# Kernel tuning notes

Hardware: AMD Instinct MI355X
Metric: run time of the kernel (lower is better)

Reference implementation:

```python
import jax, jax.numpy as jnp
import numpy as np

K = 7          # kernel_size
PAD = K // 2   # padding


def _unfold(t):
    """im2col for kxk neighborhood: (B,C,H,W) -> (B,C,K*K,H,W), zero-padded."""
    B, C, H, W = t.shape
    p = jnp.pad(t, ((0, 0), (0, 0), (PAD, PAD), (PAD, PAD)))
    # row-major over kernel offsets matches F.unfold ordering
    wins = jnp.stack([p[:, :, i:i + H, j:j + W]
                      for i in range(K) for j in range(K)], axis=2)
    return wins


def setup_inputs() -> dict:
    key = jax.random.key(0)
    ks = jax.random.split(key, 7)
    B, C, H, W = 8, 128, 64, 64
    scale = 1.0 / np.sqrt(C)
    x = jax.random.normal(ks[0], (B, C, H, W), dtype=jnp.float32)
    Wq = jax.random.normal(ks[1], (C, C), dtype=jnp.float32) * scale
    Wk = jax.random.normal(ks[2], (C, C), dtype=jnp.float32) * scale
    Wv = jax.random.normal(ks[3], (C, C), dtype=jnp.float32) * scale
    bq = jax.random.normal(ks[4], (C,), dtype=jnp.float32) * 0.01
    bk = jax.random.normal(ks[5], (C,), dtype=jnp.float32) * 0.01
    bv = jax.random.normal(ks[6], (C,), dtype=jnp.float32) * 0.01
    return {"x": x, "Wq": Wq, "bq": bq, "Wk": Wk, "bk": bk, "Wv": Wv, "bv": bv}


def reference(x, Wq, bq, Wk, bk, Wv, bv):
    # 1x1 convs = channel GEMMs
    q = jnp.einsum('oc,bchw->bohw', Wq, x) + bq[:, None, None]
    k = jnp.einsum('oc,bchw->bohw', Wk, x) + bk[:, None, None]
    v = jnp.einsum('oc,bchw->bohw', Wv, x) + bv[:, None, None]
    k_unf = _unfold(k)   # (B,C,K*K,H,W)
    v_unf = _unfold(v)   # (B,C,K*K,H,W)
    # attention scores over the K*K neighborhood, summed over channels
    attn = jnp.einsum('bchw,bcphw->bphw', q, k_unf)
    attn = jax.nn.softmax(attn, axis=1)
    y = jnp.einsum('bphw,bcphw->bchw', attn, v_unf)
    return y
```

## Files before the change

### kernel.cpp

```cpp
#include <hip/hip_runtime.h>
#include <hip/hip_bf16.h>

#define CC   128
#define HH_  64
#define WW_  64
#define BB   8
#define HWSZ (HH_*WW_)
#define CHW  (CC*HWSZ)
#define BCHW (BB*CHW)
#define PAD  3
#define NP   49

typedef __attribute__((ext_vector_type(8))) short short8;
typedef __attribute__((ext_vector_type(4))) float float4v;

__global__ __launch_bounds__(256) void prep_w(
    const float* __restrict__ Wq, const float* __restrict__ Wk,
    const float* __restrict__ Wv,
    unsigned short* __restrict__ whi, unsigned short* __restrict__ wlo)
{
    int i = blockIdx.x * 256 + threadIdx.x;
    const float* src = (i < 16384) ? Wq : (i < 32768 ? Wk : Wv);
    float f = src[i & 16383];
    __hip_bfloat16 h = __float2bfloat16(f);
    float hf = __bfloat162float(h);
    __hip_bfloat16 l = __float2bfloat16(f - hf);
    unsigned short hu, lu;
    __builtin_memcpy(&hu, &h, 2);
    __builtin_memcpy(&lu, &l, 2);
    whi[i] = hu;
    wlo[i] = lu;
}

__global__ __launch_bounds__(256, 2) void qkv_mfma(
    const float* __restrict__ x,
    const unsigned short* __restrict__ whi, const unsigned short* __restrict__ wlo,
    const float* __restrict__ bq, const float* __restrict__ bk,
    const float* __restrict__ bv, float* __restrict__ qkv)
{
    __shared__ unsigned short xT[2][128][136];
    const int proj = blockIdx.y;
    const int n0g  = blockIdx.x << 7;
    const int b    = n0g >> 12;
    const int npx  = n0g & 4095;
    const int tid  = threadIdx.x;
    const int lane = tid & 63;
    const int wv   = tid >> 6;
    const int wm   = wv & 1, wn = wv >> 1;

    const float* xb = x + (size_t)b*CHW + npx;
    #pragma unroll
    for (int it = 0; it < 16; ++it) {
        int f  = tid + (it << 8);
        int c  = f >> 5;
        int p4 = (f & 31) << 2;
        float4 v = *(const float4*)&xb[(size_t)c*HWSZ + p4];
        float vv[4] = {v.x, v.y, v.z, v.w};
        #pragma unroll
        for (int u = 0; u < 4; ++u) {
            __hip_bfloat16 h = __float2bfloat16(vv[u]);
            float hf = __bfloat162float(h);
            __hip_bfloat16 l = __float2bfloat16(vv[u] - hf);
            unsigned short hu, lu;
            __builtin_memcpy(&hu, &h, 2);
            __builtin_memcpy(&lu, &l, 2);
            xT[0][p4 + u][c] = hu;
            xT[1][p4 + u][c] = lu;
        }
    }

    const float* Bp = (proj == 0) ? bq : (proj == 1 ? bk : bv);
    const int q4 = lane >> 4;
    float4v acc[4][4];
    #pragma unroll
    for (int sm = 0; sm < 4; ++sm) {
        const int mb = wm*64 + sm*16 + q4*4;
        float4v bi;
        bi[0] = Bp[mb+0]; bi[1] = Bp[mb+1]; bi[2] = Bp[mb+2]; bi[3] = Bp[mb+3];
        #pragma unroll
        for (int sn = 0; sn < 4; ++sn) acc[sm][sn] = bi;
    }

    __syncthreads();

    const unsigned short* Wh = whi + (size_t)proj*16384;
    const unsigned short* Wl = wlo + (size_t)proj*16384;
    const int kq8  = q4 << 3;
    const int mrow = lane & 15;

    for (int pass = 0; pass < 3; ++pass) {
        const unsigned short* Wp = (pass == 2) ? Wl : Wh;
        const int xi = (pass == 1) ? 1 : 0;
        #pragma unroll
        for (int kc = 0; kc < 4; ++kc) {
            const int kb = kc << 5;
            short8 a[4], bf[4];
            #pragma unroll
            for (int sm = 0; sm < 4; ++sm) {
                const int m = wm*64 + sm*16 + mrow;
                a[sm] = *(const short8*)&Wp[(size_t)m*CC + kb + kq8];
            }
            #pragma unroll
            for (int sn = 0; sn < 4; ++sn) {
                const int n = wn*64 + sn*16 + mrow;
                bf[sn] = *(const short8*)&xT[xi][n][kb + kq8];
            }
            #pragma unroll
            for (int sm = 0; sm < 4; ++sm)
                #pragma unroll
                for (int sn = 0; sn < 4; ++sn)
                    acc[sm][sn] = __builtin_amdgcn_mfma_f32_16x16x32_bf16(
                        a[sm], bf[sn], acc[sm][sn], 0, 0, 0);
        }
    }

    float* op = qkv + (size_t)proj*BCHW + (size_t)b*CHW + npx;
    #pragma unroll
    for (int sm = 0; sm < 4; ++sm) {
        const int mb = wm*64 + sm*16 + q4*4;
        #pragma unroll
        for (int sn = 0; sn < 4; ++sn) {
            const int n = wn*64 + sn*16 + mrow;
            #pragma unroll
            for (int r = 0; r < 4; ++r)
                op[(size_t)(mb + r)*HWSZ + n] = acc[sm][sn][r];
        }
    }
}

__device__ __forceinline__ void load_chunk8(const float* __restrict__ src,
                                            int h0, int c0, float4* stg) {
    const int tid = threadIdx.x;
    #pragma unroll
    for (int i = 0; i < 4; ++i) {
        int f   = tid + (i << 9);
        int c   = f >> 7;
        int rem = f & 127;
        int r   = rem >> 4;
        int q4  = (rem & 15) << 2;
        int hh  = h0 - PAD + r;
        if ((unsigned)hh < (unsigned)HH_)
            stg[i] = *(const float4*)&src[(size_t)(c0 + c)*HWSZ + hh*WW_ + q4];
        else
            stg[i] = make_float4(0.f, 0.f, 0.f, 0.f);
    }
}

__global__ __launch_bounds__(512) void locatt(
    const float* __restrict__ qkv, float* __restrict__ out)
{
    __shared__ __align__(16) float smem[8*72*17];
    __shared__ float lg[2][NP][64];
    __shared__ float dn[2][64];

    const int blk = blockIdx.x;
    const int xs  = blk & 7;
    const int jj  = blk >> 3;
    const int b   = jj >> 2;
    const int h0  = (((xs << 2) | (jj & 3)) << 1);
    const int tid = threadIdx.x;
    const int s   = tid >> 6;
    const int lane = tid & 63;
    const int q16  = lane & 15;
    const int csub = lane >> 4;
    const int w4   = q16 << 2;
    const int w    = lane;

    const float* qp = qkv + (size_t)b*CHW;
    const float* kp = qkv + (size_t)BCHW + (size_t)b*CHW;
    const float* vp = qkv + (size_t)2*BCHW + (size_t)b*CHW;

    float (*ks)[8][72] = (float(*)[8][72])smem;

    if (tid < 256) {
        int idx = tid & 127;
        int c = idx >> 3, r = idx & 7;
        int col = (tid < 128) ? 0 : 68;
        *(float4*)&ks[c][r][col] = make_float4(0.f, 0.f, 0.f, 0.f);
    }

    const bool do0 = (s < 7);
    const bool do1 = (s >= 1);

    float acc0[7][4], acc1[7][4];
    #pragma unroll
    for (int dx = 0; dx < 7; ++dx)
        #pragma unroll
        for (int j = 0; j < 4; ++j) { acc0[dx][j] = 0.f; acc1[dx][j] = 0.f; }

    float4 stg[4];
    load_chunk8(kp, h0, 0, stg);

    for (int ck = 0; ck < 8; ++ck) {
        #pragma unroll
        for (int i = 0; i < 4; ++i) {
            int f   = tid + (i << 9);
            int c   = f >> 7;
            int rem = f & 127;
            int r   = rem >> 4;
            int q4  = (rem & 15) << 2;
            *(float4*)&ks[c][r][4 + q4] = stg[i];
        }
        __syncthreads();
        if (ck < 7) load_chunk8(kp, h0, (ck + 1) * 16, stg);

        const int c0 = ck << 4;
        #pragma unroll
        for (int ci4 = 0; ci4 < 4; ++ci4) {
            const int c = (ci4 << 2) + csub;
            const float* qc = qp + (size_t)(c0 + c)*HWSZ + h0*WW_ + w4;
            float4 q0v = do0 ? *(const float4*)qc
                             : make_float4(0.f, 0.f, 0.f, 0.f);
            float4 q1v = do1 ? *(const float4*)(qc + WW_)
                             : make_float4(0.f, 0.f, 0.f, 0.f);
            float4 ka  = *(const float4*)&ks[c][s][w4];
            float4 kb  = *(const float4*)&ks[c][s][w4 + 4];
            float4 kc2 = *(const float4*)&ks[c][s][w4 + 8];
            float kw[12] = {ka.x,ka.y,ka.z,ka.w, kb.x,kb.y,kb.z,kb.w,
                            kc2.x,kc2.y,kc2.z,kc2.w};
            float q0a[4] = {q0v.x,q0v.y,q0v.z,q0v.w};
            float q1a[4] = {q1v.x,q1v.y,q1v.z,q1v.w};
            #pragma unroll
            for (int dx = 0; dx < 7; ++dx)
                #pragma unroll
                for (int j = 0; j < 4; ++j) {
                    float kv = kw[j + dx + 1];
                    acc0[dx][j] = fmaf(q0a[j], kv, acc0[dx][j]);
                    acc1[dx][j] = fmaf(q1a[j], kv, acc1[dx][j]);
                }
        }
        __syncthreads();
    }

    #pragma unroll
    for (int dx = 0; dx < 7; ++dx)
        #pragma unroll
        for (int j = 0; j < 4; ++j) {
            acc0[dx][j] += __shfl_xor(acc0[dx][j], 16, 64);
            acc0[dx][j] += __shfl_xor(acc0[dx][j], 32, 64);
            acc1[dx][j] += __shfl_xor(acc1[dx][j], 16, 64);
            acc1[dx][j] += __shfl_xor(acc1[dx][j], 32, 64);
        }
    #pragma unroll
    for (int dx = 0; dx < 7; ++dx) {
        if ((dx & 3) == csub) {
            if (do0) *(float4*)&lg[0][s*7 + dx][w4] =
                make_float4(acc0[dx][0], acc0[dx][1], acc0[dx][2], acc0[dx][3]);
            if (do1) *(float4*)&lg[1][(s-1)*7 + dx][w4] =
                make_float4(acc1[dx][0], acc1[dx][1], acc1[dx][2], acc1[dx][3]);
        }
    }

    float vreg[16];
    {
        #pragma unroll
        for (int i = 0; i < 16; ++i) {
            int c  = 2*s + (i >> 3);
            int r  = i & 7;
            int hh = h0 - PAD + r;
            vreg[i] = ((unsigned)hh < (unsigned)HH_)
                      ? vp[(size_t)c*HWSZ + hh*WW_ + w] : 0.f;
        }
    }
    __syncthreads();

    if (tid < 128) {
        const int r = tid >> 6, px = tid & 63;
        float tv[NP];
        float m = -1e30f;
        #pragma unroll
        for (int p = 0; p < NP; ++p) { tv[p] = lg[r][p][px]; m = fmaxf(m, tv[p]); }
        float d = 0.f;
        #pragma unroll
        for (int p = 0; p < NP; ++p) {
            float e = __expf(tv[p] - m);
            d += e;
            lg[r][p][px] = e;
        }
        dn[r][px] = 1.f / d;
    } else {
        int t = tid - 128;
        for (int i = t; i < 1024; i += 384) {
            int r    = i >> 7;
            int rem  = i & 127;
            int colg = rem >> 4;
            int col  = (colg < 4) ? colg : (64 + colg);
            smem[r*1224 + col*17 + (rem & 15)] = 0.f;
        }
    }
    __syncthreads();

    float a0[NP], a1[NP];
    const float sc0 = dn[0][w], sc1 = dn[1][w];
    #pragma unroll
    for (int p = 0; p < NP; ++p) a0[p] = lg[0][p][w] * sc0;
    #pragma unroll
    for (int p = 0; p < NP; ++p) a1[p] = lg[1][p][w] * sc1;

    for (int ck = 0; ck < 8; ++ck) {
        #pragma unroll
        for (int i = 0; i < 16; ++i) {
            int c = 2*s + (i >> 3);
            int r = i & 7;
            smem[r*1224 + (4 + w)*17 + c] = vreg[i];
        }
        __syncthreads();
        if (ck < 7) {
            int c0v = (ck + 1) << 4;
            #pragma unroll
            for (int i = 0; i < 16; ++i) {
                int c  = 2*s + (i >> 3);
                int r  = i & 7;
                int hh = h0 - PAD + r;
                vreg[i] = ((unsigned)hh < (unsigned)HH_)
                          ? vp[(size_t)(c0v + c)*HWSZ + hh*WW_ + w] : 0.f;
            }
        }
        float y0a = 0.f, y0b = 0.f, y1a = 0.f, y1b = 0.f;
        #pragma unroll
        for (int r = 0; r < 8; ++r) {
            const float* vbase = &smem[r*1224 + (1 + w)*17 + 2*s];
            #pragma unroll
            for (int dx = 0; dx < 7; ++dx) {
                float va = vbase[17*dx];
                float vb = vbase[17*dx + 1];
                if (r < 7) {
                    float aw = a0[r*7 + dx];
                    y0a = fmaf(aw, va, y0a); y0b = fmaf(aw, vb, y0b);
                }
                if (r >= 1) {
                    float aw = a1[(r-1)*7 + dx];
                    y1a = fmaf(aw, va, y1a); y1b = fmaf(aw, vb, y1b);
                }
            }
        }
        float* op = out + (size_t)b*CHW + (size_t)(ck*16 + 2*s)*HWSZ
                        + (size_t)h0*WW_ + w;
        op[0]          = y0a;
        op[WW_]        = y1a;
        op[HWSZ]       = y0b;
        op[HWSZ + WW_] = y1b;
        __syncthreads();
    }
}

extern "C" void kernel_launch(void* const* d_in, const int* in_sizes, int n_in,
                              void* d_out, int out_size, void* d_ws, size_t ws_size,
                              hipStream_t stream) {
    const float* x  = (const float*)d_in[0];
    const float* Wq = (const float*)d_in[1];
    const float* bq = (const float*)d_in[2];
    const float* Wk = (const float*)d_in[3];
    const float* bk = (const float*)d_in[4];
    const float* Wv = (const float*)d_in[5];
    const float* bv = (const float*)d_in[6];
    float* out = (float*)d_out;
    float* qkv = (float*)d_ws;

    unsigned short* whi = (unsigned short*)d_out;
    unsigned short* wlo = whi + 3*16384;

    prep_w  <<<192, 256, 0, stream>>>(Wq, Wk, Wv, whi, wlo);
    qkv_mfma<<<dim3(256, 3), 256, 0, stream>>>(x, whi, wlo, bq, bk, bv, qkv);
    locatt  <<<256, 512, 0, stream>>>(qkv, out);
}
```

Baseline: 144.4 us.

## Loop projections in one QKV block and load K/V windows directly from global

The QKV GEMM now converts each x tile to split-bf16 once and loops over the three projections inside the block, instead of launching a separate block per projection. The local-attention kernel drops its LDS staging of K and V and the per-chunk barriers. Each thread instead loads 12-wide row windows straight from global memory (relying on cache), computes four channel groups per thread, and applies the softmax normalisation at the end. The weight scratch moves from the output buffer to the workspace. The trade-off is fewer blocks in the GEMM and more redundant global/L2 traffic in exchange for removing synchronisation.

```diff
diff --git a/kernel.cpp b/kernel.cpp
--- a/kernel.cpp
+++ b/kernel.cpp
@@ -32,14 +32,13 @@
     wlo[i] = lu;
 }
 
-__global__ __launch_bounds__(256, 2) void qkv_mfma(
+__global__ __launch_bounds__(256) void qkv_mfma(
     const float* __restrict__ x,
     const unsigned short* __restrict__ whi, const unsigned short* __restrict__ wlo,
     const float* __restrict__ bq, const float* __restrict__ bk,
     const float* __restrict__ bv, float* __restrict__ qkv)
 {
     __shared__ unsigned short xT[2][128][136];
-    const int proj = blockIdx.y;
     const int n0g  = blockIdx.x << 7;
     const int b    = n0g >> 12;
     const int npx  = n0g & 4095;
@@ -68,119 +67,112 @@
             xT[1][p4 + u][c] = lu;
         }
     }
-
-    const float* Bp = (proj == 0) ? bq : (proj == 1 ? bk : bv);
-    const int q4 = lane >> 4;
-    float4v acc[4][4];
-    #pragma unroll
-    for (int sm = 0; sm < 4; ++sm) {
-        const int mb = wm*64 + sm*16 + q4*4;
-        float4v bi;
-        bi[0] = Bp[mb+0]; bi[1] = Bp[mb+1]; bi[2] = Bp[mb+2]; bi[3] = Bp[mb+3];
-        #pragma unroll
-        for (int sn = 0; sn < 4; ++sn) acc[sm][sn] = bi;
-    }
-
     __syncthreads();
 
-    const unsigned short* Wh = whi + (size_t)proj*16384;
-    const unsigned short* Wl = wlo + (size_t)proj*16384;
+    const int q4   = lane >> 4;
     const int kq8  = q4 << 3;
     const int mrow = lane & 15;
 
-    for (int pass = 0; pass < 3; ++pass) {
-        const unsigned short* Wp = (pass == 2) ? Wl : Wh;
-        const int xi = (pass == 1) ? 1 : 0;
-        #pragma unroll
-        for (int kc = 0; kc < 4; ++kc) {
-            const int kb = kc << 5;
-            short8 a[4], bf[4];
-            #pragma unroll
-            for (int sm = 0; sm < 4; ++sm) {
-                const int m = wm*64 + sm*16 + mrow;
-                a[sm] = *(const short8*)&Wp[(size_t)m*CC + kb + kq8];
+    for (int proj = 0; proj < 3; ++proj) {
+        const float* Bp = (proj == 0) ? bq : (proj == 1 ? bk : bv);
+        float4v acc[4][4];
+        #pragma unroll
+        for (int sm = 0; sm < 4; ++sm) {
+            const int mb = wm*64 + sm*16 + q4*4;
+            float4v bi;
+            bi[0] = Bp[mb+0]; bi[1] = Bp[mb+1]; bi[2] = Bp[mb+2]; bi[3] = Bp[mb+3];
+            #pragma unroll
+            for (int sn = 0; sn < 4; ++sn) acc[sm][sn] = bi;
+        }
+
+        const unsigned short* Wh = whi + (size_t)proj*16384;
+        const unsigned short* Wl = wlo + (size_t)proj*16384;
+
+        #pragma unroll
+        for (int pass = 0; pass < 3; ++pass) {
+            const unsigned short* Wp = (pass == 2) ? Wl : Wh;
+            const int xi = (pass == 1) ? 1 : 0;
+            #pragma unroll
+            for (int kc = 0; kc < 4; ++kc) {
+                const int kb = kc << 5;
+                short8 a[4], bf[4];
+                #pragma unroll
+                for (int sm = 0; sm < 4; ++sm) {
+                    const int m = wm*64 + sm*16 + mrow;
+                    a[sm] = *(const short8*)&Wp[(size_t)m*CC + kb + kq8];
+                }
+                #pragma unroll
+                for (int sn = 0; sn < 4; ++sn) {
+                    const int n = wn*64 + sn*16 + mrow;
+                    bf[sn] = *(const short8*)&xT[xi][n][kb + kq8];
+                }
+                #pragma unroll
+                for (int sm = 0; sm < 4; ++sm)
+                    #pragma unroll
+                    for (int sn = 0; sn < 4; ++sn)
+                        acc[sm][sn] = __builtin_amdgcn_mfma_f32_16x16x32_bf16(
+                            a[sm], bf[sn], acc[sm][sn], 0, 0, 0);
             }
+        }
+
+        float* op = qkv + (size_t)proj*BCHW + (size_t)b*CHW + npx;
+        #pragma unroll
+        for (int sm = 0; sm < 4; ++sm) {
+            const int mb = wm*64 + sm*16 + q4*4;
             #pragma unroll
             for (int sn = 0; sn < 4; ++sn) {
                 const int n = wn*64 + sn*16 + mrow;
-                bf[sn] = *(const short8*)&xT[xi][n][kb + kq8];
+                #pragma unroll
+                for (int r = 0; r < 4; ++r)
+                    op[(size_t)(mb + r)*HWSZ + n] = acc[sm][sn][r];
             }
-            #pragma unroll
-            for (int sm = 0; sm < 4; ++sm)
-                #pragma unroll
-                for (int sn = 0; sn < 4; ++sn)
-                    acc[sm][sn] = __builtin_amdgcn_mfma_f32_16x16x32_bf16(
-                        a[sm], bf[sn], acc[sm][sn], 0, 0, 0);
-        }
-    }
-
-    float* op = qkv + (size_t)proj*BCHW + (size_t)b*CHW + npx;
-    #pragma unroll
-    for (int sm = 0; sm < 4; ++sm) {
-        const int mb = wm*64 + sm*16 + q4*4;
-        #pragma unroll
-        for (int sn = 0; sn < 4; ++sn) {
-            const int n = wn*64 + sn*16 + mrow;
-            #pragma unroll
-            for (int r = 0; r < 4; ++r)
-                op[(size_t)(mb + r)*HWSZ + n] = acc[sm][sn][r];
-        }
-    }
-}
-
-__device__ __forceinline__ void load_chunk8(const float* __restrict__ src,
-                                            int h0, int c0, float4* stg) {
-    const int tid = threadIdx.x;
-    #pragma unroll
-    for (int i = 0; i < 4; ++i) {
-        int f   = tid + (i << 9);
-        int c   = f >> 7;
-        int rem = f & 127;
-        int r   = rem >> 4;
-        int q4  = (rem & 15) << 2;
-        int hh  = h0 - PAD + r;
-        if ((unsigned)hh < (unsigned)HH_)
-            stg[i] = *(const float4*)&src[(size_t)(c0 + c)*HWSZ + hh*WW_ + q4];
-        else
-            stg[i] = make_float4(0.f, 0.f, 0.f, 0.f);
-    }
+        }
+    }
+}
+
+__device__ __forceinline__ void win12(const float* __restrict__ rowp,
+                                      bool rv, int q16, float* kw) {
+    float4 a, b, c;
+    if (rv) {
+        a = *(const float4*)(rowp - 4);
+        b = *(const float4*)(rowp);
+        c = *(const float4*)(rowp + 4);
+        if (q16 == 0)  { a.x = a.y = a.z = a.w = 0.f; }
+        if (q16 == 15) { c.x = c.y = c.z = c.w = 0.f; }
+    } else {
+        a = b = c = make_float4(0.f, 0.f, 0.f, 0.f);
+    }
+    kw[0]=a.x; kw[1]=a.y; kw[2]=a.z;  kw[3]=a.w;
+    kw[4]=b.x; kw[5]=b.y; kw[6]=b.z;  kw[7]=b.w;
+    kw[8]=c.x; kw[9]=c.y; kw[10]=c.z; kw[11]=c.w;
 }
 
 __global__ __launch_bounds__(512) void locatt(
     const float* __restrict__ qkv, float* __restrict__ out)
 {
-    __shared__ __align__(16) float smem[8*72*17];
     __shared__ float lg[2][NP][64];
     __shared__ float dn[2][64];
 
     const int blk = blockIdx.x;
-    const int xs  = blk & 7;
+    const int xsw = blk & 7;
     const int jj  = blk >> 3;
     const int b   = jj >> 2;
-    const int h0  = (((xs << 2) | (jj & 3)) << 1);
-    const int tid = threadIdx.x;
-    const int s   = tid >> 6;
+    const int h0  = (((xsw << 2) | (jj & 3)) << 1);
+    const int tid  = threadIdx.x;
+    const int s    = tid >> 6;
     const int lane = tid & 63;
     const int q16  = lane & 15;
     const int csub = lane >> 4;
     const int w4   = q16 << 2;
-    const int w    = lane;
 
     const float* qp = qkv + (size_t)b*CHW;
     const float* kp = qkv + (size_t)BCHW + (size_t)b*CHW;
     const float* vp = qkv + (size_t)2*BCHW + (size_t)b*CHW;
 
-    float (*ks)[8][72] = (float(*)[8][72])smem;
-
-    if (tid < 256) {
-        int idx = tid & 127;
-        int c = idx >> 3, r = idx & 7;
-        int col = (tid < 128) ? 0 : 68;
-        *(float4*)&ks[c][r][col] = make_float4(0.f, 0.f, 0.f, 0.f);
-    }
-
     const bool do0 = (s < 7);
     const bool do1 = (s >= 1);
+    const int  hhk = h0 - PAD + s;
+    const bool kv_ok = (unsigned)hhk < (unsigned)HH_;
 
     float acc0[7][4], acc1[7][4];
     #pragma unroll
@@ -188,48 +180,29 @@
         #pragma unroll
         for (int j = 0; j < 4; ++j) { acc0[dx][j] = 0.f; acc1[dx][j] = 0.f; }
 
-    float4 stg[4];
-    load_chunk8(kp, h0, 0, stg);
-
     for (int ck = 0; ck < 8; ++ck) {
-        #pragma unroll
-        for (int i = 0; i < 4; ++i) {
-            int f   = tid + (i << 9);
-            int c   = f >> 7;
-            int rem = f & 127;
-            int r   = rem >> 4;
-            int q4  = (rem & 15) << 2;
-            *(float4*)&ks[c][r][4 + q4] = stg[i];
-        }
-        __syncthreads();
-        if (ck < 7) load_chunk8(kp, h0, (ck + 1) * 16, stg);
-
         const int c0 = ck << 4;
         #pragma unroll
         for (int ci4 = 0; ci4 < 4; ++ci4) {
-            const int c = (ci4 << 2) + csub;
-            const float* qc = qp + (size_t)(c0 + c)*HWSZ + h0*WW_ + w4;
+            const int c = c0 + (ci4 << 2) + csub;
+            float kw[12];
+            win12(kp + (size_t)c*HWSZ + (long)hhk*WW_ + w4, kv_ok, q16, kw);
+            const float* qc = qp + (size_t)c*HWSZ + h0*WW_ + w4;
             float4 q0v = do0 ? *(const float4*)qc
                              : make_float4(0.f, 0.f, 0.f, 0.f);
             float4 q1v = do1 ? *(const float4*)(qc + WW_)
                              : make_float4(0.f, 0.f, 0.f, 0.f);
-            float4 ka  = *(const float4*)&ks[c][s][w4];
-            float4 kb  = *(const float4*)&ks[c][s][w4 + 4];
-            float4 kc2 = *(const float4*)&ks[c][s][w4 + 8];
-            float kw[12] = {ka.x,ka.y,ka.z,ka.w, kb.x,kb.y,kb.z,kb.w,
-                            kc2.x,kc2.y,kc2.z,kc2.w};
-            float q0a[4] = {q0v.x,q0v.y,q0v.z,q0v.w};
-            float q1a[4] = {q1v.x,q1v.y,q1v.z,q1v.w};
+            float q0a[4] = {q0v.x, q0v.y, q0v.z, q0v.w};
+            float q1a[4] = {q1v.x, q1v.y, q1v.z, q1v.w};
             #pragma unroll
             for (int dx = 0; dx < 7; ++dx)
                 #pragma unroll
                 for (int j = 0; j < 4; ++j) {
-                    float kv = kw[j + dx + 1];
-                    acc0[dx][j] = fmaf(q0a[j], kv, acc0[dx][j]);
-                    acc1[dx][j] = fmaf(q1a[j], kv, acc1[dx][j]);
+                    float kvv = kw[j + dx + 1];
+                    acc0[dx][j] = fmaf(q0a[j], kvv, acc0[dx][j]);
+                    acc1[dx][j] = fmaf(q1a[j], kvv, acc1[dx][j]);
                 }
         }
-        __syncthreads();
     }
 
     #pragma unroll
@@ -250,18 +223,6 @@
                 make_float4(acc1[dx][0], acc1[dx][1], acc1[dx][2], acc1[dx][3]);
         }
     }
-
-    float vreg[16];
-    {
-        #pragma unroll
-        for (int i = 0; i < 16; ++i) {
-            int c  = 2*s + (i >> 3);
-            int r  = i & 7;
-            int hh = h0 - PAD + r;
-            vreg[i] = ((unsigned)hh < (unsigned)HH_)
-                      ? vp[(size_t)c*HWSZ + hh*WW_ + w] : 0.f;
-        }
-    }
     __syncthreads();
 
     if (tid < 128) {
@@ -278,69 +239,62 @@
             lg[r][p][px] = e;
         }
         dn[r][px] = 1.f / d;
-    } else {
-        int t = tid - 128;
-        for (int i = t; i < 1024; i += 384) {
-            int r    = i >> 7;
-            int rem  = i & 127;
-            int colg = rem >> 4;
-            int col  = (colg < 4) ? colg : (64 + colg);
-            smem[r*1224 + col*17 + (rem & 15)] = 0.f;
-        }
     }
     __syncthreads();
 
-    float a0[NP], a1[NP];
-    const float sc0 = dn[0][w], sc1 = dn[1][w];
-    #pragma unroll
-    for (int p = 0; p < NP; ++p) a0[p] = lg[0][p][w] * sc0;
-    #pragma unroll
-    for (int p = 0; p < NP; ++p) a1[p] = lg[1][p][w] * sc1;
-
-    for (int ck = 0; ck < 8; ++ck) {
-        #pragma unroll
-        for (int i = 0; i < 16; ++i) {
-            int c = 2*s + (i >> 3);
-            int r = i & 7;
-            smem[r*1224 + (4 + w)*17 + c] = vreg[i];
-        }
-        __syncthreads();
-        if (ck < 7) {
-            int c0v = (ck + 1) << 4;
-            #pragma unroll
-            for (int i = 0; i < 16; ++i) {
-                int c  = 2*s + (i >> 3);
-                int r  = i & 7;
-                int hh = h0 - PAD + r;
-                vreg[i] = ((unsigned)hh < (unsigned)HH_)
-                          ? vp[(size_t)(c0v + c)*HWSZ + hh*WW_ + w] : 0.f;
+    float y0[4][4], y1[4][4];
+    #pragma unroll
+    for (int cg = 0; cg < 4; ++cg)
+        #pragma unroll
+        for (int j = 0; j < 4; ++j) { y0[cg][j] = 0.f; y1[cg][j] = 0.f; }
+
+    const int cbase = (s << 2) + csub;
+    #pragma unroll
+    for (int r = 0; r < 8; ++r) {
+        const int hh = h0 - PAD + r;
+        const bool rv = (unsigned)hh < (unsigned)HH_;
+        float vw[4][12];
+        #pragma unroll
+        for (int cg = 0; cg < 4; ++cg) {
+            const int c = (cg << 5) + cbase;
+            win12(vp + (size_t)c*HWSZ + (long)hh*WW_ + w4, rv, q16, vw[cg]);
+        }
+        #pragma unroll
+        for (int dx = 0; dx < 7; ++dx) {
+            float a0a[4], a1a[4];
+            if (r < 7) {
+                float4 aq = *(const float4*)&lg[0][r*7 + dx][w4];
+                a0a[0]=aq.x; a0a[1]=aq.y; a0a[2]=aq.z; a0a[3]=aq.w;
             }
-        }
-        float y0a = 0.f, y0b = 0.f, y1a = 0.f, y1b = 0.f;
-        #pragma unroll
-        for (int r = 0; r < 8; ++r) {
-            const float* vbase = &smem[r*1224 + (1 + w)*17 + 2*s];
-            #pragma unroll
-            for (int dx = 0; dx < 7; ++dx) {
-                float va = vbase[17*dx];
-                float vb = vbase[17*dx + 1];
-                if (r < 7) {
-                    float aw = a0[r*7 + dx];
-                    y0a = fmaf(aw, va, y0a); y0b = fmaf(aw, vb, y0b);
+            if (r >= 1) {
+                float4 aq = *(const float4*)&lg[1][(r-1)*7 + dx][w4];
+                a1a[0]=aq.x; a1a[1]=aq.y; a1a[2]=aq.z; a1a[3]=aq.w;
+            }
+            #pragma unroll
+            for (int cg = 0; cg < 4; ++cg)
+                #pragma unroll
+                for (int j = 0; j < 4; ++j) {
+                    float vv = vw[cg][j + dx + 1];
+                    if (r < 7)  y0[cg][j] = fmaf(a0a[j], vv, y0[cg][j]);
+                    if (r >= 1) y1[cg][j] = fmaf(a1a[j], vv, y1[cg][j]);
                 }
-                if (r >= 1) {
-                    float aw = a1[(r-1)*7 + dx];
-                    y1a = fmaf(aw, va, y1a); y1b = fmaf(aw, vb, y1b);
-                }
-            }
-        }
-        float* op = out + (size_t)b*CHW + (size_t)(ck*16 + 2*s)*HWSZ
-                        + (size_t)h0*WW_ + w;
-        op[0]          = y0a;
-        op[WW_]        = y1a;
-        op[HWSZ]       = y0b;
-        op[HWSZ + WW_] = y1b;
-        __syncthreads();
+        }
+    }
+
+    const float4 s0v = *(const float4*)&dn[0][w4];
+    const float4 s1v = *(const float4*)&dn[1][w4];
+    const float s0a[4] = {s0v.x, s0v.y, s0v.z, s0v.w};
+    const float s1a[4] = {s1v.x, s1v.y, s1v.z, s1v.w};
+    #pragma unroll
+    for (int cg = 0; cg < 4; ++cg) {
+        const int c = (cg << 5) + cbase;
+        float* op = out + (size_t)b*CHW + (size_t)c*HWSZ + (size_t)h0*WW_ + w4;
+        float4 o0 = make_float4(y0[cg][0]*s0a[0], y0[cg][1]*s0a[1],
+                                y0[cg][2]*s0a[2], y0[cg][3]*s0a[3]);
+        float4 o1 = make_float4(y1[cg][0]*s1a[0], y1[cg][1]*s1a[1],
+                                y1[cg][2]*s1a[2], y1[cg][3]*s1a[3]);
+        *(float4*)op         = o0;
+        *(float4*)(op + WW_) = o1;
     }
 }
 
@@ -356,11 +310,10 @@
     const float* bv = (const float*)d_in[6];
     float* out = (float*)d_out;
     float* qkv = (float*)d_ws;
-
-    unsigned short* whi = (unsigned short*)d_out;
+    unsigned short* whi = (unsigned short*)(qkv + (size_t)3*BCHW);
     unsigned short* wlo = whi + 3*16384;
 
     prep_w  <<<192, 256, 0, stream>>>(Wq, Wk, Wv, whi, wlo);
-    qkv_mfma<<<dim3(256, 3), 256, 0, stream>>>(x, whi, wlo, bq, bk, bv, qkv);
+    qkv_mfma<<<256, 256, 0, stream>>>(x, whi, wlo, bq, bk, bv, qkv);
     locatt  <<<256, 512, 0, stream>>>(qkv, out);
 }
```

Result: slower. 305.6 us (+111.7%).
